# Kernel optimization log

Hardware: AMD Instinct MI355X
Metric: run time of the kernel (lower is better)

The kernel has to match this reference:

```python
import jax, jax.numpy as jnp
import numpy as np

N_NODES = 100000
N_EDGES = 1600000
N_GRAPHS = 512
IN_DIM = 64
HID = 64
OUT_DIM = 2


def setup_inputs() -> dict:
    key = jax.random.key(0)
    ks = jax.random.split(key, 8)
    x = jax.random.normal(ks[0], (N_NODES, IN_DIM), dtype=jnp.float32)
    edge_index = jax.random.randint(ks[1], (2, N_EDGES), 0, N_NODES, dtype=jnp.int64)
    batch = jnp.sort(jax.random.randint(ks[2], (N_NODES,), 0, N_GRAPHS, dtype=jnp.int64))
    s1 = 1.0 / np.sqrt(IN_DIM)
    s2 = 1.0 / np.sqrt(HID)
    W1 = jax.random.normal(ks[3], (IN_DIM, HID), dtype=jnp.float32) * s1
    b1 = jnp.zeros((HID,), dtype=jnp.float32)
    W2 = jax.random.normal(ks[4], (HID, HID), dtype=jnp.float32) * s2
    b2 = jnp.zeros((HID,), dtype=jnp.float32)
    Wfc = jax.random.normal(ks[5], (HID, OUT_DIM), dtype=jnp.float32) * s2
    bfc = jnp.zeros((OUT_DIM,), dtype=jnp.float32)
    return {"x": x, "edge_index": edge_index, "batch": batch,
            "W1": W1, "b1": b1, "W2": W2, "b2": b2, "Wfc": Wfc, "bfc": bfc}


def _gcn_conv(x, src, dst, dinv, W, b):
    # PyG GCNConv: h = D^{-1/2}(A+I)D^{-1/2} X W + b, self-loops already in src/dst
    h = x @ W  # [N, H]
    norm = dinv[src] * dinv[dst]  # [E+N]
    msg = h[src] * norm[:, None]  # gather over edges
    return jax.ops.segment_sum(msg, dst, num_segments=N_NODES) + b


def reference(x, edge_index, batch, W1, b1, W2, b2, Wfc, bfc):
    loops = jnp.arange(N_NODES, dtype=edge_index.dtype)
    src = jnp.concatenate([edge_index[0], loops])
    dst = jnp.concatenate([edge_index[1], loops])
    deg = jax.ops.segment_sum(jnp.ones_like(dst, dtype=x.dtype), dst, num_segments=N_NODES)
    dinv = jnp.where(deg > 0, jax.lax.rsqrt(jnp.maximum(deg, 1.0)), 0.0)
    h = jax.nn.relu(_gcn_conv(x, src, dst, dinv, W1, b1))
    h = jax.nn.relu(_gcn_conv(h, src, dst, dinv, W2, b2))
    # global mean pool over graphs
    sums = jax.ops.segment_sum(h, batch, num_segments=N_GRAPHS)
    cnts = jax.ops.segment_sum(jnp.ones((N_NODES,), dtype=h.dtype), batch, num_segments=N_GRAPHS)
    pooled = sums / jnp.maximum(cnts, 1.0)[:, None]
    return pooled @ Wfc + bfc
```

## Files before the change

### kernel.cpp

```cpp
#include <hip/hip_runtime.h>

#define NN 100000
#define NE 1600000
#define NG 512
#define FD 64
#define NSL 4
#define CHUNK 128
#define SCAN_CHUNK 1024
#define SCAN_BLOCKS 98

__device__ inline unsigned pack_bf16x2(float a, float b) {
    unsigned ua = __float_as_uint(a), ub = __float_as_uint(b);
    ua = (ua + 0x7FFFu + ((ua >> 16) & 1u)) >> 16;
    ub = (ub + 0x7FFFu + ((ub >> 16) & 1u)) >> 16;
    return ua | (ub << 16);
}
__device__ inline float bf_lo(unsigned u) { return __uint_as_float(u << 16); }
__device__ inline float bf_hi(unsigned u) { return __uint_as_float(u & 0xFFFF0000u); }


__global__ void k_count_rank(const int* __restrict__ dst, int* __restrict__ cnt,
                             int* __restrict__ rank, int e) {
    int i = blockIdx.x * 256 + threadIdx.x;
    if (i < e) rank[i] = atomicAdd(&cnt[dst[i]], 1);
}

__global__ void k_scan1(const int* __restrict__ cnt, int* __restrict__ part,
                        int* __restrict__ blockSum, int n) {
    __shared__ int lds[256];
    int tid = threadIdx.x;
    int base = blockIdx.x * SCAN_CHUNK + tid * 4;
    int v0 = (base + 0 < n) ? cnt[base + 0] : 0;
    int v1 = (base + 1 < n) ? cnt[base + 1] : 0;
    int v2 = (base + 2 < n) ? cnt[base + 2] : 0;
    int v3 = (base + 3 < n) ? cnt[base + 3] : 0;
    int s = v0 + v1 + v2 + v3;
    lds[tid] = s;
    __syncthreads();
    for (int off = 1; off < 256; off <<= 1) {
        int t = (tid >= off) ? lds[tid - off] : 0;
        __syncthreads();
        lds[tid] += t;
        __syncthreads();
    }
    int run = lds[tid] - s;
    if (base + 0 < n) part[base + 0] = run; run += v0;
    if (base + 1 < n) part[base + 1] = run; run += v1;
    if (base + 2 < n) part[base + 2] = run; run += v2;
    if (base + 3 < n) part[base + 3] = run;
    if (tid == 255) blockSum[blockIdx.x] = lds[255];
}

__global__ void k_scan2(const int* __restrict__ bs, int* __restrict__ boff, int nb) {
    __shared__ int lds[128];
    int tid = threadIdx.x;
    int v = (tid < nb) ? bs[tid] : 0;
    lds[tid] = v;
    __syncthreads();
    for (int off = 1; off < 128; off <<= 1) {
        int t = (tid >= off) ? lds[tid - off] : 0;
        __syncthreads();
        lds[tid] += t;
        __syncthreads();
    }
    if (tid < nb) boff[tid] = lds[tid] - v;
}

__global__ void k_scan3(int* __restrict__ rowptr, const int* __restrict__ boff,
                        const int* __restrict__ cnt, float* __restrict__ dinv, int n) {
    int i = blockIdx.x * 256 + threadIdx.x;
    if (i < n) {
        rowptr[i] = rowptr[i] + boff[i >> 10];
        float deg = (float)(cnt[i] + 1);
        dinv[i] = 1.0f / sqrtf(deg);
    }
}

__global__ void k_pcnt_bs(const int* __restrict__ batch, int* __restrict__ pcnt, int n, int ng) {
    int g = blockIdx.x * 256 + threadIdx.x;
    if (g >= ng) return;
    int lo = 0, hi = n;
    while (lo < hi) { int m = (lo + hi) >> 1; if (batch[m] < g) lo = m + 1; else hi = m; }
    int l0 = lo;
    lo = 0; hi = n;
    int v = g + 1;
    while (lo < hi) { int m = (lo + hi) >> 1; if (batch[m] < v) lo = m + 1; else hi = m; }
    pcnt[g] = lo - l0;
}

__global__ void k_fill(const int* __restrict__ src, const int* __restrict__ dst,
                       const int* __restrict__ rank, const int* __restrict__ rowptr,
                       int* __restrict__ colidx, int e) {
    int i = blockIdx.x * 256 + threadIdx.x;
    if (i < e) {
        int d = dst[i];
        colidx[rowptr[d] + rank[i]] = src[i];
    }
}

__global__ void k_gemm_scale(const float* __restrict__ in, const float* __restrict__ W,
                             const float* __restrict__ dinv, unsigned* __restrict__ hs, int n) {
    __shared__ float w[FD * FD];
    __shared__ float xr[4][4][80];
    int tid = threadIdx.x;
    {
        const float4* W4 = (const float4*)W;
        float4* w4s = (float4*)w;
        for (int i = tid; i < FD * FD / 4; i += 256) w4s[i] = W4[i];
    }
    int wave = tid >> 6, lane = tid & 63;
    int r = lane >> 4;
    int c = lane & 15;
    int row = blockIdx.x * 16 + wave * 4 + r;
    bool valid = row < n;
    if (valid) {
        float4 xv = ((const float4*)in)[row * 16 + c];
        *((float4*)&xr[wave][r][c * 4]) = xv;
    }
    __syncthreads();
    if (!valid) return;
    const float4* w4 = (const float4*)w;
    float4 acc = {0.f, 0.f, 0.f, 0.f};
#pragma unroll
    for (int k = 0; k < FD; ++k) {
        float xv = xr[wave][r][k];
        float4 wv = w4[k * 16 + c];
        acc.x = fmaf(xv, wv.x, acc.x);
        acc.y = fmaf(xv, wv.y, acc.y);
        acc.z = fmaf(xv, wv.z, acc.z);
        acc.w = fmaf(xv, wv.w, acc.w);
    }
    float d = dinv[row];
    uint2 o;
    o.x = pack_bf16x2(acc.x * d, acc.y * d);
    o.y = pack_bf16x2(acc.z * d, acc.w * d);
    ((uint2*)hs)[((size_t)(c >> 2) * NN + row) * 4 + (c & 3)] = o;
}

template <int POOL>
__global__ void k_agg4(const unsigned* __restrict__ hs, const int* __restrict__ rowptr,
                       const int* __restrict__ cnt, const int* __restrict__ colidx,
                       const float* __restrict__ dinv, const float* __restrict__ b,
                       const int* __restrict__ batch, float* __restrict__ outp, int n) {
    int bid = blockIdx.x;
    int s = bid & 3;
    int chunk = bid >> 2;
    int tid = threadIdx.x;
    int wave = tid >> 6, lane = tid & 63;
    int slot = lane >> 3, fp = lane & 7;
    const unsigned* S = hs + (size_t)s * NN * 8;
    float b0 = b[s * 16 + fp * 2], b1 = b[s * 16 + fp * 2 + 1];
    int node = chunk * CHUNK + wave;
    if (node >= n) return;
    int rs = rowptr[node], ct = cnt[node];
    float dv = dinv[node];
    int bg = POOL ? batch[node] : 0;
    int c0 = colidx[rs + slot];
    int c1 = colidx[rs + 8 + slot];
    for (int t = 0; t < CHUNK / 4; ++t) {
        bool ok0 = slot < ct, ok1 = slot + 8 < ct;
        int i0 = ok0 ? c0 : node;
        int i1 = ok1 ? c1 : node;
        unsigned w0 = S[(size_t)i0 * 8 + fp];
        unsigned w1 = S[(size_t)i1 * 8 + fp];
        unsigned sv = S[(size_t)node * 8 + fp];
        int node2 = node + 4;
        int ncl = node2 < n ? node2 : n - 1;
        int rs2 = rowptr[ncl], ct2 = cnt[ncl];
        float dv2 = dinv[ncl];
        int bg2 = POOL ? batch[ncl] : 0;
        int c0n = colidx[rs2 + slot];
        int c1n = colidx[rs2 + 8 + slot];
        w0 = ok0 ? w0 : 0u;
        w1 = ok1 ? w1 : 0u;
        float a0 = bf_lo(w0) + bf_lo(w1);
        float a1 = bf_hi(w0) + bf_hi(w1);
        int e = rs + ct;
        for (int i = rs + 16; i < e; i += 8) {
            int cc = colidx[i + slot];
            bool ok = (i + slot) < e;
            int ii = ok ? cc : node;
            unsigned ww = S[(size_t)ii * 8 + fp];
            ww = ok ? ww : 0u;
            a0 += bf_lo(ww);
            a1 += bf_hi(ww);
        }
        a0 += __shfl_xor(a0, 8, 64);  a1 += __shfl_xor(a1, 8, 64);
        a0 += __shfl_xor(a0, 16, 64); a1 += __shfl_xor(a1, 16, 64);
        a0 += __shfl_xor(a0, 32, 64); a1 += __shfl_xor(a1, 32, 64);
        if (lane < 8) {
            float t0 = a0 + bf_lo(sv), t1 = a1 + bf_hi(sv);
            float r0 = fmaxf(fmaf(t0, dv, b0), 0.f);
            float r1 = fmaxf(fmaf(t1, dv, b1), 0.f);
            if (POOL) {
                float* p = &outp[((size_t)s * NG + bg) * 16 + fp * 2];
                atomicAdd(p + 0, r0);
                atomicAdd(p + 1, r1);
            } else {
                float2 o = {r0, r1};
                *(float2*)(outp + (size_t)node * FD + s * 16 + fp * 2) = o;
            }
        }
        node = node2;
        if (node >= n) break;
        rs = rs2; ct = ct2; dv = dv2; bg = bg2; c0 = c0n; c1 = c1n;
    }
}

__global__ void k_final(const float* __restrict__ pool, const int* __restrict__ pcnt,
                        const float* __restrict__ Wfc, const float* __restrict__ bfc,
                        float* __restrict__ out, int ng) {
    int tid = threadIdx.x;
    int wave = tid >> 6, lane = tid & 63;
    int g = blockIdx.x * 4 + wave;
    if (g >= ng) return;
    float inv = 1.0f / fmaxf((float)pcnt[g], 1.0f);
    float s = pool[((size_t)(lane >> 4) * NG + g) * 16 + (lane & 15)] * inv;
    float a0 = s * Wfc[lane * 2 + 0];
    float a1 = s * Wfc[lane * 2 + 1];
#pragma unroll
    for (int off = 32; off > 0; off >>= 1) {
        a0 += __shfl_down(a0, off, 64);
        a1 += __shfl_down(a1, off, 64);
    }
    if (lane == 0) {
        out[g * 2 + 0] = a0 + bfc[0];
        out[g * 2 + 1] = a1 + bfc[1];
    }
}

extern "C" void kernel_launch(void* const* d_in, const int* in_sizes, int n_in,
                              void* d_out, int out_size, void* d_ws, size_t ws_size,
                              hipStream_t stream) {
    const float* x    = (const float*)d_in[0];
    const int*   eidx = (const int*)d_in[1];
    const int*   batch= (const int*)d_in[2];
    const float* W1   = (const float*)d_in[3];
    const float* b1   = (const float*)d_in[4];
    const float* W2   = (const float*)d_in[5];
    const float* b2   = (const float*)d_in[6];
    const float* Wfc  = (const float*)d_in[7];
    const float* bfc  = (const float*)d_in[8];
    float* out = (float*)d_out;

    const int* esrc = eidx;
    const int* edst = eidx + NE;

    char* ws = (char*)d_ws;
    size_t off = 0;
    auto alloc = [&](size_t bytes) {
        char* p = ws + off;
        off += (bytes + 255) & ~(size_t)255;
        return p;
    };
    int*      cnt      = (int*)     alloc(NN * 4);
    int*      rowptr   = (int*)     alloc(NN * 4);
    int*      blockSum = (int*)     alloc(128 * 4);
    int*      blockOff = (int*)     alloc(128 * 4);
    float*    dinv     = (float*)   alloc(NN * 4);
    int*      colidx   = (int*)     alloc((size_t)(NE + 64) * 4);
    unsigned* hs       = (unsigned*)alloc((size_t)NN * FD * 2);
    float*    h1       = (float*)   alloc((size_t)NN * FD * 4);
    float*    pool     = (float*)   alloc((size_t)NSL * NG * 16 * 4);
    int*      pcnt     = (int*)     alloc(NG * 4);
    int*      rank     = (int*)h1;
    (void)ws_size;

    hipMemsetAsync(cnt,  0, NN * 4, stream);
    hipMemsetAsync(pool, 0, (size_t)NSL * NG * 16 * 4, stream);

    const int GE = (NE + 255) / 256;
    const int GN = (NN + 255) / 256;
    const int GR = (NN + 15) / 16;
    const int GA = ((NN + CHUNK - 1) / CHUNK) * NSL;

    k_count_rank<<<GE, 256, 0, stream>>>(edst, cnt, rank, NE);
    k_scan1<<<SCAN_BLOCKS, 256, 0, stream>>>(cnt, rowptr, blockSum, NN);
    k_scan2<<<1, 128, 0, stream>>>(blockSum, blockOff, SCAN_BLOCKS);
    k_scan3<<<GN, 256, 0, stream>>>(rowptr, blockOff, cnt, dinv, NN);
    k_pcnt_bs<<<2, 256, 0, stream>>>(batch, pcnt, NN, NG);
    k_fill<<<GE, 256, 0, stream>>>(esrc, edst, rank, rowptr, colidx, NE);

    k_gemm_scale<<<GR, 256, 0, stream>>>(x, W1, dinv, hs, NN);
    k_agg4<0><<<GA, 256, 0, stream>>>(hs, rowptr, cnt, colidx, dinv, b1, batch, h1, NN);

    k_gemm_scale<<<GR, 256, 0, stream>>>(h1, W2, dinv, hs, NN);
    k_agg4<1><<<GA, 256, 0, stream>>>(hs, rowptr, cnt, colidx, dinv, b2, batch, pool, NN);

    k_final<<<(NG + 3) / 4, 256, 0, stream>>>(pool, pcnt, Wfc, bfc, out, NG);
}
```

Baseline: 404.7 us.

## Pad CSR rows to 16 with sentinel node, unroll gather, store h1 as bf16

```diff
diff --git a/kernel.cpp b/kernel.cpp
--- a/kernel.cpp
+++ b/kernel.cpp
@@ -8,6 +8,8 @@
 #define CHUNK 128
 #define SCAN_CHUNK 1024
 #define SCAN_BLOCKS 98
+#define SR (NN + 1)
+#define COLCAP (NE + 15 * NN + 64)
 
 __device__ inline unsigned pack_bf16x2(float a, float b) {
     unsigned ua = __float_as_uint(a), ub = __float_as_uint(b);
@@ -18,6 +20,27 @@
 __device__ inline float bf_lo(unsigned u) { return __uint_as_float(u << 16); }
 __device__ inline float bf_hi(unsigned u) { return __uint_as_float(u & 0xFFFF0000u); }
 
+__global__ void k_init(int* __restrict__ colidx, int* __restrict__ cnt,
+                       float* __restrict__ pool, unsigned* __restrict__ hs) {
+    int i = blockIdx.x * 256 + threadIdx.x;
+    if (i < COLCAP / 4) {
+        int4 v = {NN, NN, NN, NN};
+        ((int4*)colidx)[i] = v;
+    }
+    if (i < NN / 4) {
+        int4 z = {0, 0, 0, 0};
+        ((int4*)cnt)[i] = z;
+    }
+    if (i < NSL * NG * 16 / 4) {
+        float4 z = {0.f, 0.f, 0.f, 0.f};
+        ((float4*)pool)[i] = z;
+    }
+    if (i < 8) {
+        uint4 z = {0u, 0u, 0u, 0u};
+        ((uint4*)hs)[((size_t)(i >> 1) * SR + NN) * 2 + (i & 1)] = z;
+    }
+}
+
 
 __global__ void k_count_rank(const int* __restrict__ dst, int* __restrict__ cnt,
                              int* __restrict__ rank, int e) {
@@ -30,10 +53,10 @@
     __shared__ int lds[256];
     int tid = threadIdx.x;
     int base = blockIdx.x * SCAN_CHUNK + tid * 4;
-    int v0 = (base + 0 < n) ? cnt[base + 0] : 0;
-    int v1 = (base + 1 < n) ? cnt[base + 1] : 0;
-    int v2 = (base + 2 < n) ? cnt[base + 2] : 0;
-    int v3 = (base + 3 < n) ? cnt[base + 3] : 0;
+    int v0 = (base + 0 < n) ? (cnt[base + 0] + 15) & ~15 : 0;
+    int v1 = (base + 1 < n) ? (cnt[base + 1] + 15) & ~15 : 0;
+    int v2 = (base + 2 < n) ? (cnt[base + 2] + 15) & ~15 : 0;
+    int v3 = (base + 3 < n) ? (cnt[base + 3] + 15) & ~15 : 0;
     int s = v0 + v1 + v2 + v3;
     lds[tid] = s;
     __syncthreads();
@@ -98,7 +121,8 @@
     }
 }
 
-__global__ void k_gemm_scale(const float* __restrict__ in, const float* __restrict__ W,
+template <int BF16IN>
+__global__ void k_gemm_scale(const void* __restrict__ inv_, const float* __restrict__ W,
                              const float* __restrict__ dinv, unsigned* __restrict__ hs, int n) {
     __shared__ float w[FD * FD];
     __shared__ float xr[4][4][80];
@@ -114,8 +138,16 @@
     int row = blockIdx.x * 16 + wave * 4 + r;
     bool valid = row < n;
     if (valid) {
-        float4 xv = ((const float4*)in)[row * 16 + c];
-        *((float4*)&xr[wave][r][c * 4]) = xv;
+        if (BF16IN) {
+            uint2 v = ((const uint2*)inv_)[((size_t)(c >> 2) * NN + row) * 4 + (c & 3)];
+            xr[wave][r][c * 4 + 0] = bf_lo(v.x);
+            xr[wave][r][c * 4 + 1] = bf_hi(v.x);
+            xr[wave][r][c * 4 + 2] = bf_lo(v.y);
+            xr[wave][r][c * 4 + 3] = bf_hi(v.y);
+        } else {
+            float4 xv = ((const float4*)inv_)[row * 16 + c];
+            *((float4*)&xr[wave][r][c * 4]) = xv;
+        }
     }
     __syncthreads();
     if (!valid) return;
@@ -134,21 +166,21 @@
     uint2 o;
     o.x = pack_bf16x2(acc.x * d, acc.y * d);
     o.y = pack_bf16x2(acc.z * d, acc.w * d);
-    ((uint2*)hs)[((size_t)(c >> 2) * NN + row) * 4 + (c & 3)] = o;
+    ((uint2*)hs)[((size_t)(c >> 2) * SR + row) * 4 + (c & 3)] = o;
 }
 
 template <int POOL>
 __global__ void k_agg4(const unsigned* __restrict__ hs, const int* __restrict__ rowptr,
                        const int* __restrict__ cnt, const int* __restrict__ colidx,
                        const float* __restrict__ dinv, const float* __restrict__ b,
-                       const int* __restrict__ batch, float* __restrict__ outp, int n) {
+                       const int* __restrict__ batch, void* __restrict__ outp, int n) {
     int bid = blockIdx.x;
     int s = bid & 3;
     int chunk = bid >> 2;
     int tid = threadIdx.x;
     int wave = tid >> 6, lane = tid & 63;
     int slot = lane >> 3, fp = lane & 7;
-    const unsigned* S = hs + (size_t)s * NN * 8;
+    const unsigned* S = hs + (size_t)s * SR * 8;
     float b0 = b[s * 16 + fp * 2], b1 = b[s * 16 + fp * 2 + 1];
     int node = chunk * CHUNK + wave;
     if (node >= n) return;
@@ -157,33 +189,41 @@
     int bg = POOL ? batch[node] : 0;
     int c0 = colidx[rs + slot];
     int c1 = colidx[rs + 8 + slot];
+    int c2 = colidx[rs + 16 + slot];
+    int c3 = colidx[rs + 24 + slot];
     for (int t = 0; t < CHUNK / 4; ++t) {
-        bool ok0 = slot < ct, ok1 = slot + 8 < ct;
-        int i0 = ok0 ? c0 : node;
-        int i1 = ok1 ? c1 : node;
-        unsigned w0 = S[(size_t)i0 * 8 + fp];
-        unsigned w1 = S[(size_t)i1 * 8 + fp];
+        unsigned w0 = S[(size_t)c0 * 8 + fp];
+        unsigned w1 = S[(size_t)c1 * 8 + fp];
         unsigned sv = S[(size_t)node * 8 + fp];
         int node2 = node + 4;
         int ncl = node2 < n ? node2 : n - 1;
         int rs2 = rowptr[ncl], ct2 = cnt[ncl];
         float dv2 = dinv[ncl];
         int bg2 = POOL ? batch[ncl] : 0;
-        int c0n = colidx[rs2 + slot];
-        int c1n = colidx[rs2 + 8 + slot];
-        w0 = ok0 ? w0 : 0u;
-        w1 = ok1 ? w1 : 0u;
-        float a0 = bf_lo(w0) + bf_lo(w1);
-        float a1 = bf_hi(w0) + bf_hi(w1);
-        int e = rs + ct;
-        for (int i = rs + 16; i < e; i += 8) {
-            int cc = colidx[i + slot];
-            bool ok = (i + slot) < e;
-            int ii = ok ? cc : node;
-            unsigned ww = S[(size_t)ii * 8 + fp];
-            ww = ok ? ww : 0u;
-            a0 += bf_lo(ww);
-            a1 += bf_hi(ww);
+        int nc0 = colidx[rs2 + slot];
+        int nc1 = colidx[rs2 + 8 + slot];
+        int nc2 = colidx[rs2 + 16 + slot];
+        int nc3 = colidx[rs2 + 24 + slot];
+        float a0 = 0.f, a1 = 0.f;
+        if (ct > 0) {
+            a0 = bf_lo(w0) + bf_lo(w1);
+            a1 = bf_hi(w0) + bf_hi(w1);
+            if (ct > 16) {
+                unsigned w2 = S[(size_t)c2 * 8 + fp];
+                unsigned w3 = S[(size_t)c3 * 8 + fp];
+                a0 += bf_lo(w2) + bf_lo(w3);
+                a1 += bf_hi(w2) + bf_hi(w3);
+                if (ct > 32) {
+                    int e = rs + ((ct + 15) & ~15);
+                    for (int i = rs + 32; i < e; i += 16) {
+                        int x0 = colidx[i + slot], x1 = colidx[i + 8 + slot];
+                        unsigned y0 = S[(size_t)x0 * 8 + fp];
+                        unsigned y1 = S[(size_t)x1 * 8 + fp];
+                        a0 += bf_lo(y0) + bf_lo(y1);
+                        a1 += bf_hi(y0) + bf_hi(y1);
+                    }
+                }
+            }
         }
         a0 += __shfl_xor(a0, 8, 64);  a1 += __shfl_xor(a1, 8, 64);
         a0 += __shfl_xor(a0, 16, 64); a1 += __shfl_xor(a1, 16, 64);
@@ -193,17 +233,17 @@
             float r0 = fmaxf(fmaf(t0, dv, b0), 0.f);
             float r1 = fmaxf(fmaf(t1, dv, b1), 0.f);
             if (POOL) {
-                float* p = &outp[((size_t)s * NG + bg) * 16 + fp * 2];
+                float* p = &((float*)outp)[((size_t)s * NG + bg) * 16 + fp * 2];
                 atomicAdd(p + 0, r0);
                 atomicAdd(p + 1, r1);
             } else {
-                float2 o = {r0, r1};
-                *(float2*)(outp + (size_t)node * FD + s * 16 + fp * 2) = o;
+                ((unsigned*)outp)[((size_t)s * NN + node) * 8 + fp] = pack_bf16x2(r0, r1);
             }
         }
         node = node2;
         if (node >= n) break;
-        rs = rs2; ct = ct2; dv = dv2; bg = bg2; c0 = c0n; c1 = c1n;
+        rs = rs2; ct = ct2; dv = dv2; bg = bg2;
+        c0 = nc0; c1 = nc1; c2 = nc2; c3 = nc3;
     }
 }
 
@@ -258,22 +298,21 @@
     int*      blockSum = (int*)     alloc(128 * 4);
     int*      blockOff = (int*)     alloc(128 * 4);
     float*    dinv     = (float*)   alloc(NN * 4);
-    int*      colidx   = (int*)     alloc((size_t)(NE + 64) * 4);
-    unsigned* hs       = (unsigned*)alloc((size_t)NN * FD * 2);
-    float*    h1       = (float*)   alloc((size_t)NN * FD * 4);
+    int*      colidx   = (int*)     alloc((size_t)COLCAP * 4);
+    unsigned* hs       = (unsigned*)alloc((size_t)SR * FD * 2);
+    unsigned* h1       = (unsigned*)alloc((size_t)NN * FD * 2);
     float*    pool     = (float*)   alloc((size_t)NSL * NG * 16 * 4);
     int*      pcnt     = (int*)     alloc(NG * 4);
     int*      rank     = (int*)h1;
     (void)ws_size;
 
-    hipMemsetAsync(cnt,  0, NN * 4, stream);
-    hipMemsetAsync(pool, 0, (size_t)NSL * NG * 16 * 4, stream);
-
     const int GE = (NE + 255) / 256;
     const int GN = (NN + 255) / 256;
     const int GR = (NN + 15) / 16;
     const int GA = ((NN + CHUNK - 1) / CHUNK) * NSL;
-
+    const int GI = (COLCAP / 4 + 255) / 256;
+
+    k_init<<<GI, 256, 0, stream>>>(colidx, cnt, pool, hs);
     k_count_rank<<<GE, 256, 0, stream>>>(edst, cnt, rank, NE);
     k_scan1<<<SCAN_BLOCKS, 256, 0, stream>>>(cnt, rowptr, blockSum, NN);
     k_scan2<<<1, 128, 0, stream>>>(blockSum, blockOff, SCAN_BLOCKS);
@@ -281,10 +320,10 @@
     k_pcnt_bs<<<2, 256, 0, stream>>>(batch, pcnt, NN, NG);
     k_fill<<<GE, 256, 0, stream>>>(esrc, edst, rank, rowptr, colidx, NE);
 
-    k_gemm_scale<<<GR, 256, 0, stream>>>(x, W1, dinv, hs, NN);
+    k_gemm_scale<0><<<GR, 256, 0, stream>>>(x, W1, dinv, hs, NN);
     k_agg4<0><<<GA, 256, 0, stream>>>(hs, rowptr, cnt, colidx, dinv, b1, batch, h1, NN);
 
-    k_gemm_scale<<<GR, 256, 0, stream>>>(h1, W2, dinv, hs, NN);
+    k_gemm_scale<1><<<GR, 256, 0, stream>>>(h1, W2, dinv, hs, NN);
     k_agg4<1><<<GA, 256, 0, stream>>>(hs, rowptr, cnt, colidx, dinv, b2, batch, pool, NN);
 
     k_final<<<(NG + 3) / 4, 256, 0, stream>>>(pool, pcnt, Wfc, bfc, out, NG);
```

Result: slower. 425.2 us (+5.1%).
